# Performance work log

Measured on AMD Instinct MI355X. Metric: run time of the kernel, lower is better.

Reference implementation:

```python
import jax, jax.numpy as jnp
import numpy as np

H = 256
K = 16
EPS_LN = 1e-5


def setup_inputs() -> dict:
    key = jax.random.key(0)
    ks = jax.random.split(key, 24)
    B, N = 64, 256
    s = lambda *sh: 1.0 / np.sqrt(sh[0])
    inp = {
        "feat": jax.random.normal(ks[0], (B, N, H), jnp.float32),
        "centers": jax.random.normal(ks[1], (B, N, 3), jnp.float32),
        "text_global": jax.random.normal(ks[2], (B, H), jnp.float32),
        # geom_mlp: Linear(4,H) -> ReLU -> Linear(H,H) -> ReLU
        "w_geom1": jax.random.normal(ks[3], (4, H), jnp.float32) * s(4),
        "b_geom1": jnp.zeros((H,), jnp.float32),
        "w_geom2": jax.random.normal(ks[4], (H, H), jnp.float32) * s(H),
        "b_geom2": jnp.zeros((H,), jnp.float32),
        # text gate / bias projections
        "w_gate": jax.random.normal(ks[5], (H, H), jnp.float32) * s(H),
        "b_gate": jnp.zeros((H,), jnp.float32),
        "w_tbias": jax.random.normal(ks[6], (H, H), jnp.float32) * s(H),
        "b_tbias": jnp.zeros((H,), jnp.float32),
        # edge_mlp: Linear(H,H//2) -> ReLU -> Linear(H//2,1)
        "w_edge1": jax.random.normal(ks[7], (H, H // 2), jnp.float32) * s(H),
        "b_edge1": jnp.zeros((H // 2,), jnp.float32),
        "w_edge2": jax.random.normal(ks[8], (H // 2, 1), jnp.float32) * s(H // 2),
        "b_edge2": jnp.zeros((1,), jnp.float32),
        # msg_mlp: Linear(H,H) -> ReLU
        "w_msg": jax.random.normal(ks[9], (H, H), jnp.float32) * s(H),
        "b_msg": jnp.zeros((H,), jnp.float32),
        # out_proj: Linear(2H,H) -> ReLU
        "w_out": jax.random.normal(ks[10], (2 * H, H), jnp.float32) * s(2 * H),
        "b_out": jnp.zeros((H,), jnp.float32),
        # LayerNorm params
        "ln_gamma": jnp.ones((H,), jnp.float32),
        "ln_beta": jnp.zeros((H,), jnp.float32),
    }
    return inp


def _forward(feat, centers, text_global,
             w_geom1, b_geom1, w_geom2, b_geom2,
             w_gate, b_gate, w_tbias, b_tbias,
             w_edge1, b_edge1, w_edge2, b_edge2,
             w_msg, b_msg, w_out, b_out, ln_gamma, ln_beta):
    B, N, Hd = feat.shape
    k = min(K, N)
    # pairwise euclidean distances (B,N,N)
    sq = jnp.sum(centers * centers, axis=-1)  # (B,N)
    d2 = sq[:, :, None] + sq[:, None, :] - 2.0 * jnp.einsum('bnc,bmc->bnm', centers, centers)
    dist_matrix = jnp.sqrt(jnp.maximum(d2, 0.0))
    # k smallest -> top_k of negated distances (sorted ascending in distance)
    _, knn_idx = jax.lax.top_k(-dist_matrix, k)  # (B,N,k)
    idx_flat = knn_idx.reshape(B, N * k)
    feat_neigh = jnp.take_along_axis(feat, idx_flat[:, :, None], axis=1).reshape(B, N, k, Hd)
    centers_neigh = jnp.take_along_axis(centers, idx_flat[:, :, None], axis=1).reshape(B, N, k, 3)
    rel = centers_neigh - centers[:, :, None, :]  # (B,N,k,3)
    dist = jnp.linalg.norm(rel, axis=-1, keepdims=True) + 1e-6
    geom = jnp.concatenate([rel, jnp.log1p(dist)], axis=-1)  # (B,N,k,4)
    geom_emb = jax.nn.relu(jax.nn.relu(geom @ w_geom1 + b_geom1) @ w_geom2 + b_geom2)
    text_gate = jax.nn.sigmoid(text_global @ w_gate + b_gate)[:, None, None, :]
    text_bias = (text_global @ w_tbias + b_tbias)[:, None, None, :]
    geom_cond = geom_emb * text_gate + text_bias
    edge_feat = jnp.tanh(feat[:, :, None, :] + feat_neigh + geom_cond)  # (B,N,k,H)
    edge_logits = (jax.nn.relu(edge_feat @ w_edge1 + b_edge1) @ w_edge2 + b_edge2)[..., 0]
    edge_alpha = jax.nn.softmax(edge_logits, axis=-1)[..., None]  # (B,N,k,1)
    msg = jax.nn.relu(feat_neigh @ w_msg + b_msg)
    ctx = jnp.sum(edge_alpha * msg, axis=2)  # (B,N,H)
    out = jax.nn.relu(jnp.concatenate([feat, ctx], axis=-1) @ w_out + b_out)
    x = feat + out
    mu = jnp.mean(x, axis=-1, keepdims=True)
    var = jnp.mean((x - mu) ** 2, axis=-1, keepdims=True)
    return (x - mu) / jnp.sqrt(var + EPS_LN) * ln_gamma + ln_beta


def reference(feat, centers, text_global,
              w_geom1, b_geom1, w_geom2, b_geom2,
              w_gate, b_gate, w_tbias, b_tbias,
              w_edge1, b_edge1, w_edge2, b_edge2,
              w_msg, b_msg, w_out, b_out, ln_gamma, ln_beta):
    return _forward(feat, centers, text_global,
                    w_geom1, b_geom1, w_geom2, b_geom2,
                    w_gate, b_gate, w_tbias, b_tbias,
                    w_edge1, b_edge1, w_edge2, b_edge2,
                    w_msg, b_msg, w_out, b_out, ln_gamma, ln_beta)
```

## Files before the change

kernel.cpp:

```cpp
#include <hip/hip_runtime.h>

#define H 256
#define KNN 16
#define NPT 256
#define BB 64

typedef unsigned short u16;
typedef unsigned int u32;
typedef __attribute__((ext_vector_type(8))) short shortx8;
typedef __attribute__((ext_vector_type(4))) float floatx4;

__device__ __forceinline__ u16 f2b(float f) {
    u32 u = __float_as_uint(f);
    u32 r = (u + 0x7fffu + ((u >> 16) & 1u)) >> 16;
    return (u16)r;
}

__device__ __forceinline__ float fast_tanh(float x) {
    float e = __builtin_amdgcn_exp2f(x * 2.88539008177793f);
    return 1.0f - 2.0f * __builtin_amdgcn_rcpf(e + 1.0f);
}

__global__ __launch_bounds__(256) void prep_kernel(
    const float* __restrict__ w2, const float* __restrict__ we1,
    const float* __restrict__ wm, const float* __restrict__ wo,
    u16* __restrict__ w2t, u16* __restrict__ we1t,
    u16* __restrict__ wmt, u16* __restrict__ wot) {
    int tid = blockIdx.x * 256 + threadIdx.x;
    if (tid < 65536) {
        int n = tid >> 8, k = tid & 255;
        w2t[tid] = f2b(w2[k * 256 + n]);
    } else if (tid < 98304) {
        int t = tid - 65536;
        int n = t >> 8, k = t & 255;
        we1t[t] = f2b(we1[k * 128 + n]);
    } else if (tid < 163840) {
        int t = tid - 98304;
        int n = t >> 8, k = t & 255;
        wmt[t] = f2b(wm[k * 256 + n]);
    } else if (tid < 294912) {
        int t = tid - 163840;
        int n = t >> 9, k = t & 511;
        wot[t] = f2b(wo[k * 256 + n]);
    }
}

__global__ __launch_bounds__(256) void knn_kernel(const float* __restrict__ centers,
                                                  int* __restrict__ knn) {
    __shared__ float cx[NPT], cy[NPT], cz[NPT], sq[NPT];
    __shared__ float dl[4][64][17];
    __shared__ int il[4][64][17];
    int blk = blockIdx.x;
    int b = blk >> 2, n0 = (blk & 3) * 64;
    int h = threadIdx.x;
    int s = h >> 6, pt = h & 63;
    {
        const float* cb = centers + (size_t)b * NPT * 3;
        float x = cb[h * 3 + 0], y = cb[h * 3 + 1], z = cb[h * 3 + 2];
        cx[h] = x; cy[h] = y; cz[h] = z;
        sq[h] = x * x + y * y + z * z;
    }
    __syncthreads();
    int n = n0 + pt;
    float x = cx[n], y = cy[n], z = cz[n], sn = sq[n];
    float bd[KNN];
    int bi[KNN];
#pragma unroll
    for (int j = 0; j < KNN; j++) { bd[j] = 1e30f; bi[j] = 0x7fffffff; }
    for (int mm = 0; mm < 64; mm++) {
        int m = s * 64 + mm;
        float dot = x * cx[m] + y * cy[m] + z * cz[m];
        float d2 = (sn + sq[m]) - 2.0f * dot;
        float d = sqrtf(fmaxf(d2, 0.0f));
        if (d < bd[KNN - 1]) {
            bd[KNN - 1] = d; bi[KNN - 1] = m;
#pragma unroll
            for (int p = KNN - 1; p > 0; --p) {
                if (bd[p - 1] > bd[p]) {
                    float td = bd[p - 1]; bd[p - 1] = bd[p]; bd[p] = td;
                    int ti = bi[p - 1]; bi[p - 1] = bi[p]; bi[p] = ti;
                }
            }
        }
    }
#pragma unroll
    for (int j = 0; j < KNN; j++) { dl[s][pt][j] = bd[j]; il[s][pt][j] = bi[j]; }
    __syncthreads();
    if (s == 0) {
        float md[KNN];
        int mi[KNN];
#pragma unroll
        for (int j = 0; j < KNN; j++) { md[j] = dl[0][pt][j]; mi[j] = il[0][pt][j]; }
        for (int t = 1; t < 4; t++) {
            for (int j = 0; j < KNN; j++) {
                float d = dl[t][pt][j];
                int idx = il[t][pt][j];
                bool ins = (d < md[KNN - 1]) || (d == md[KNN - 1] && idx < mi[KNN - 1]);
                if (!ins) break;
                md[KNN - 1] = d; mi[KNN - 1] = idx;
#pragma unroll
                for (int p = KNN - 1; p > 0; --p) {
                    bool sw = (md[p - 1] > md[p]) ||
                              (md[p - 1] == md[p] && mi[p - 1] > mi[p]);
                    if (sw) {
                        float td = md[p - 1]; md[p - 1] = md[p]; md[p] = td;
                        int ti = mi[p - 1]; mi[p - 1] = mi[p]; mi[p] = ti;
                    }
                }
            }
        }
        int* kp = knn + (b * NPT + n0 + pt) * KNN;
#pragma unroll
        for (int j = 0; j < KNN; j++) kp[j] = mi[j];
    }
}

__global__ __launch_bounds__(512) void gate_kernel(const float* __restrict__ tg_g,
                                                   const float* __restrict__ wg,
                                                   const float* __restrict__ bg,
                                                   const float* __restrict__ wtb,
                                                   const float* __restrict__ btb,
                                                   float* __restrict__ gate,
                                                   float* __restrict__ tbias) {
    __shared__ float tg[H];
    int b = blockIdx.x, t = threadIdx.x;
    if (t < H) tg[t] = tg_g[b * H + t];
    __syncthreads();
    int h = t & 255;
    if (t < H) {
        float ag = bg[h];
#pragma unroll 4
        for (int i = 0; i < H; i++) ag += tg[i] * wg[i * H + h];
        gate[b * H + h] = 1.0f / (1.0f + expf(-ag));
    } else {
        float ab = btb[h];
#pragma unroll 4
        for (int i = 0; i < H; i++) ab += tg[i] * wtb[i * H + h];
        tbias[b * H + h] = ab;
    }
}

__global__ __launch_bounds__(256, 4) void msg_mfma(const float* __restrict__ feat,
                                                   const u16* __restrict__ wmt,
                                                   const float* __restrict__ bm,
                                                   float* __restrict__ MSG) {
    __shared__ __attribute__((aligned(16))) u16 A[64][264];
    int p0 = blockIdx.x * 64, h = threadIdx.x;
    int w = h >> 6, lane = h & 63, quad = lane >> 4, lq = lane & 15;
#pragma unroll 8
    for (int row = 0; row < 64; row++)
        A[row][h] = f2b(feat[(size_t)(p0 + row) * H + h]);
    __syncthreads();
    floatx4 acc[4][4];
#pragma unroll
    for (int rt = 0; rt < 4; rt++)
#pragma unroll
        for (int ct = 0; ct < 4; ct++) acc[rt][ct] = (floatx4){0, 0, 0, 0};
#pragma unroll 2
    for (int kt = 0; kt < 8; kt++) {
        shortx8 bf[4];
#pragma unroll
        for (int ct = 0; ct < 4; ct++)
            bf[ct] = *(const shortx8*)&wmt[(w * 64 + ct * 16 + lq) * 256 + kt * 32 + quad * 8];
#pragma unroll
        for (int rt = 0; rt < 4; rt++) {
            shortx8 a = *(const shortx8*)&A[rt * 16 + lq][kt * 32 + quad * 8];
#pragma unroll
            for (int ct = 0; ct < 4; ct++)
                acc[rt][ct] = __builtin_amdgcn_mfma_f32_16x16x32_bf16(a, bf[ct], acc[rt][ct], 0, 0, 0);
        }
    }
#pragma unroll
    for (int ct = 0; ct < 4; ct++) {
        int col = w * 64 + ct * 16 + lq;
        float bmc = bm[col];
#pragma unroll
        for (int rt = 0; rt < 4; rt++)
#pragma unroll
            for (int r = 0; r < 4; r++) {
                int row = rt * 16 + quad * 4 + r;
                MSG[(size_t)(p0 + row) * H + col] = fmaxf(acc[rt][ct][r] + bmc, 0.0f);
            }
    }
}

__global__ __launch_bounds__(256, 4) void edge_mfma(
    const float* __restrict__ feat, const float* __restrict__ centers,
    const float* __restrict__ w1, const float* __restrict__ b1,
    const u16* __restrict__ w2t, const float* __restrict__ b2v,
    const u16* __restrict__ we1t, const float* __restrict__ be1,
    const float* __restrict__ we2, const float* __restrict__ be2,
    const int* __restrict__ knn, const float* __restrict__ gateG,
    const float* __restrict__ tbiasG, const float* __restrict__ MSG,
    float* __restrict__ ctxG) {
    __shared__ __attribute__((aligned(16))) u16 A[64][264];
    __shared__ float fnS[4][H];
    __shared__ __attribute__((aligned(16))) float geomS[64][4];
    __shared__ int nidxS[64];
    __shared__ float part[4][64];
    __shared__ float logitsS[64];
    __shared__ float alphaS[64];

    int bn0 = blockIdx.x * 4;
    int b = bn0 >> 8, n0 = bn0 & 255;
    int h = threadIdx.x;
    int w = h >> 6, lane = h & 63, quad = lane >> 4, lq = lane & 15;

    if (h < 64) nidxS[h] = knn[bn0 * KNN + h];
#pragma unroll
    for (int p = 0; p < 4; p++)
        fnS[p][h] = feat[(size_t)(bn0 + p) * H + h];
    __syncthreads();

    if (h < 64) {
        int p = h >> 4;
        int m = nidxS[h];
        int n = n0 + p;
        const float* cb = centers + (size_t)b * NPT * 3;
        float rx = cb[m * 3 + 0] - cb[n * 3 + 0];
        float ry = cb[m * 3 + 1] - cb[n * 3 + 1];
        float rz = cb[m * 3 + 2] - cb[n * 3 + 2];
        float dist = sqrtf(rx * rx + ry * ry + rz * rz) + 1e-6f;
        geomS[h][0] = rx; geomS[h][1] = ry; geomS[h][2] = rz;
        geomS[h][3] = log1pf(dist);
    }
    __syncthreads();

    {
        float c0 = w1[h], c1 = w1[H + h], c2 = w1[2 * H + h], c3 = w1[3 * H + h];
        float bb = b1[h];
#pragma unroll 8
        for (int row = 0; row < 64; row++) {
            float4 g = *(const float4*)&geomS[row][0];
            float v = fmaxf(bb + g.x * c0 + g.y * c1 + g.z * c2 + g.w * c3, 0.0f);
            A[row][h] = f2b(v);
        }
    }
    __syncthreads();

    floatx4 acc[4][4];
#pragma unroll
    for (int rt = 0; rt < 4; rt++)
#pragma unroll
        for (int ct = 0; ct < 4; ct++) acc[rt][ct] = (floatx4){0, 0, 0, 0};
#pragma unroll 2
    for (int kt = 0; kt < 8; kt++) {
        shortx8 bf[4];
#pragma unroll
        for (int ct = 0; ct < 4; ct++)
            bf[ct] = *(const shortx8*)&w2t[(w * 64 + ct * 16 + lq) * 256 + kt * 32 + quad * 8];
#pragma unroll
        for (int rt = 0; rt < 4; rt++) {
            shortx8 a = *(const shortx8*)&A[rt * 16 + lq][kt * 32 + quad * 8];
#pragma unroll
            for (int ct = 0; ct < 4; ct++)
                acc[rt][ct] = __builtin_amdgcn_mfma_f32_16x16x32_bf16(a, bf[ct], acc[rt][ct], 0, 0, 0);
        }
    }
    __syncthreads();

#pragma unroll
    for (int ct = 0; ct < 4; ct++) {
        int col = w * 64 + ct * 16 + lq;
        float b2c = b2v[col];
        float gc = gateG[b * H + col];
        float tc = tbiasG[b * H + col];
#pragma unroll
        for (int rt = 0; rt < 4; rt++) {
            float fnc = fnS[rt][col];
#pragma unroll
            for (int r = 0; r < 4; r++) {
                int row = rt * 16 + quad * 4 + r;
                float fb = feat[((size_t)b * NPT + nidxS[row]) * H + col];
                float emb = fmaxf(acc[rt][ct][r] + b2c, 0.0f);
                float ef = fast_tanh(fnc + fb + emb * gc + tc);
                A[row][col] = f2b(ef);
            }
        }
    }
    __syncthreads();

    floatx4 acc2[4][2];
#pragma unroll
    for (int rt = 0; rt < 4; rt++)
#pragma unroll
        for (int c2 = 0; c2 < 2; c2++) acc2[rt][c2] = (floatx4){0, 0, 0, 0};
#pragma unroll 2
    for (int kt = 0; kt < 8; kt++) {
        shortx8 bf[2];
#pragma unroll
        for (int c2 = 0; c2 < 2; c2++)
            bf[c2] = *(const shortx8*)&we1t[(w * 32 + c2 * 16 + lq) * 256 + kt * 32 + quad * 8];
#pragma unroll
        for (int rt = 0; rt < 4; rt++) {
            shortx8 a = *(const shortx8*)&A[rt * 16 + lq][kt * 32 + quad * 8];
#pragma unroll
            for (int c2 = 0; c2 < 2; c2++)
                acc2[rt][c2] = __builtin_amdgcn_mfma_f32_16x16x32_bf16(a, bf[c2], acc2[rt][c2], 0, 0, 0);
        }
    }

    float pl[4][4];
#pragma unroll
    for (int rt = 0; rt < 4; rt++)
#pragma unroll
        for (int r = 0; r < 4; r++) pl[rt][r] = 0.0f;
#pragma unroll
    for (int c2 = 0; c2 < 2; c2++) {
        int col = w * 32 + c2 * 16 + lq;
        float be1c = be1[col], w2c = we2[col];
#pragma unroll
        for (int rt = 0; rt < 4; rt++)
#pragma unroll
            for (int r = 0; r < 4; r++)
                pl[rt][r] += fmaxf(acc2[rt][c2][r] + be1c, 0.0f) * w2c;
    }
#pragma unroll
    for (int d = 1; d < 16; d <<= 1)
#pragma unroll
        for (int rt = 0; rt < 4; rt++)
#pragma unroll
            for (int r = 0; r < 4; r++) pl[rt][r] += __shfl_xor(pl[rt][r], d, 16);
    if (lq == 0) {
#pragma unroll
        for (int rt = 0; rt < 4; rt++)
#pragma unroll
            for (int r = 0; r < 4; r++)
                part[w][rt * 16 + quad * 4 + r] = pl[rt][r];
    }
    __syncthreads();
    if (h < 64)
        logitsS[h] = part[0][h] + part[1][h] + part[2][h] + part[3][h] + be2[0];
    __syncthreads();
    if (h < 64) {
        int base = (h >> 4) * 16;
        float mx = -1e30f;
#pragma unroll
        for (int j = 0; j < KNN; j++) mx = fmaxf(mx, logitsS[base + j]);
        float sum = 0.0f;
#pragma unroll
        for (int j = 0; j < KNN; j++) sum += expf(logitsS[base + j] - mx);
        alphaS[h] = expf(logitsS[h] - mx) / sum;
    }
    __syncthreads();

    float c[4] = {0, 0, 0, 0};
#pragma unroll 16
    for (int row = 0; row < 64; row++) {
        float al = alphaS[row];
        c[row >> 4] += al * MSG[((size_t)b * NPT + nidxS[row]) * H + h];
    }
#pragma unroll
    for (int p = 0; p < 4; p++)
        ctxG[(size_t)(bn0 + p) * H + h] = c[p];
}

__global__ __launch_bounds__(256, 4) void out_mfma(const float* __restrict__ feat,
                                                   const float* __restrict__ ctxG,
                                                   const u16* __restrict__ wot,
                                                   const float* __restrict__ bo,
                                                   const float* __restrict__ gamma,
                                                   const float* __restrict__ beta,
                                                   float* __restrict__ out) {
    __shared__ __attribute__((aligned(16))) u16 A[32][520];
    __shared__ float redS[4][32], redS2[4][32];
    int p0 = blockIdx.x * 32, h = threadIdx.x;
    int w = h >> 6, lane = h & 63, quad = lane >> 4, lq = lane & 15;
#pragma unroll 8
    for (int row = 0; row < 32; row++) {
        A[row][h]       = f2b(feat[(size_t)(p0 + row) * H + h]);
        A[row][256 + h] = f2b(ctxG[(size_t)(p0 + row) * H + h]);
    }
    __syncthreads();
    floatx4 acc[2][4];
#pragma unroll
    for (int rt = 0; rt < 2; rt++)
#pragma unroll
        for (int ct = 0; ct < 4; ct++) acc[rt][ct] = (floatx4){0, 0, 0, 0};
#pragma unroll 2
    for (int kt = 0; kt < 16; kt++) {
        shortx8 bf[4];
#pragma unroll
        for (int ct = 0; ct < 4; ct++)
            bf[ct] = *(const shortx8*)&wot[(w * 64 + ct * 16 + lq) * 512 + kt * 32 + quad * 8];
#pragma unroll
        for (int rt = 0; rt < 2; rt++) {
            shortx8 a = *(const shortx8*)&A[rt * 16 + lq][kt * 32 + quad * 8];
#pragma unroll
            for (int ct = 0; ct < 4; ct++)
                acc[rt][ct] = __builtin_amdgcn_mfma_f32_16x16x32_bf16(a, bf[ct], acc[rt][ct], 0, 0, 0);
        }
    }
    float x[2][4][4];
    float sm[2][4], sq2[2][4];
#pragma unroll
    for (int rt = 0; rt < 2; rt++)
#pragma unroll
        for (int r = 0; r < 4; r++) { sm[rt][r] = 0.0f; sq2[rt][r] = 0.0f; }
#pragma unroll
    for (int rt = 0; rt < 2; rt++)
#pragma unroll
        for (int ct = 0; ct < 4; ct++) {
            int col = w * 64 + ct * 16 + lq;
            float boc = bo[col];
#pragma unroll
            for (int r = 0; r < 4; r++) {
                int row = rt * 16 + quad * 4 + r;
                float xx = feat[(size_t)(p0 + row) * H + col] +
                           fmaxf(acc[rt][ct][r] + boc, 0.0f);
                x[rt][ct][r] = xx;
                sm[rt][r] += xx;
                sq2[rt][r] += xx * xx;
            }
        }
#pragma unroll
    for (int d = 1; d < 16; d <<= 1)
#pragma unroll
        for (int rt = 0; rt < 2; rt++)
#pragma unroll
            for (int r = 0; r < 4; r++) {
                sm[rt][r] += __shfl_xor(sm[rt][r], d, 16);
                sq2[rt][r] += __shfl_xor(sq2[rt][r], d, 16);
            }
    if (lq == 0) {
#pragma unroll
        for (int rt = 0; rt < 2; rt++)
#pragma unroll
            for (int r = 0; r < 4; r++) {
                redS[w][rt * 16 + quad * 4 + r] = sm[rt][r];
                redS2[w][rt * 16 + quad * 4 + r] = sq2[rt][r];
            }
    }
    __syncthreads();
#pragma unroll
    for (int rt = 0; rt < 2; rt++)
#pragma unroll
        for (int r = 0; r < 4; r++) {
            int row = rt * 16 + quad * 4 + r;
            float s1 = redS[0][row] + redS[1][row] + redS[2][row] + redS[3][row];
            float s2 = redS2[0][row] + redS2[1][row] + redS2[2][row] + redS2[3][row];
            float mu = s1 * (1.0f / H);
            float var = s2 * (1.0f / H) - mu * mu;
            float inv = rsqrtf(fmaxf(var, 0.0f) + 1e-5f);
#pragma unroll
            for (int ct = 0; ct < 4; ct++) {
                int col = w * 64 + ct * 16 + lq;
                out[(size_t)(p0 + row) * H + col] =
                    (x[rt][ct][r] - mu) * inv * gamma[col] + beta[col];
            }
        }
}

extern "C" void kernel_launch(void* const* d_in, const int* in_sizes, int n_in,
                              void* d_out, int out_size, void* d_ws, size_t ws_size,
                              hipStream_t stream) {
    const float* feat    = (const float*)d_in[0];
    const float* centers = (const float*)d_in[1];
    const float* textg   = (const float*)d_in[2];
    const float* w1      = (const float*)d_in[3];
    const float* b1      = (const float*)d_in[4];
    const float* w2      = (const float*)d_in[5];
    const float* b2      = (const float*)d_in[6];
    const float* wg      = (const float*)d_in[7];
    const float* bg      = (const float*)d_in[8];
    const float* wtb     = (const float*)d_in[9];
    const float* btb     = (const float*)d_in[10];
    const float* we1     = (const float*)d_in[11];
    const float* be1     = (const float*)d_in[12];
    const float* we2     = (const float*)d_in[13];
    const float* be2     = (const float*)d_in[14];
    const float* wm      = (const float*)d_in[15];
    const float* bm      = (const float*)d_in[16];
    const float* wo      = (const float*)d_in[17];
    const float* bo      = (const float*)d_in[18];
    const float* gamma   = (const float*)d_in[19];
    const float* beta    = (const float*)d_in[20];

    char* ws = (char*)d_ws;
    size_t off = 0;
    int* knn     = (int*)(ws + off);   off += (size_t)BB * NPT * KNN * 4;
    float* gate  = (float*)(ws + off); off += (size_t)BB * H * 4;
    float* tbias = (float*)(ws + off); off += (size_t)BB * H * 4;
    float* MSG   = (float*)(ws + off); off += (size_t)BB * NPT * H * 4;
    float* ctxG  = (float*)(ws + off); off += (size_t)BB * NPT * H * 4;
    u16* w2t     = (u16*)(ws + off);   off += (size_t)256 * 256 * 2;
    u16* we1t    = (u16*)(ws + off);   off += (size_t)128 * 256 * 2;
    u16* wmt     = (u16*)(ws + off);   off += (size_t)256 * 256 * 2;
    u16* wot     = (u16*)(ws + off);   off += (size_t)256 * 512 * 2;

    prep_kernel<<<1152, 256, 0, stream>>>(w2, we1, wm, wo, w2t, we1t, wmt, wot);
    knn_kernel<<<256, 256, 0, stream>>>(centers, knn);
    gate_kernel<<<BB, 512, 0, stream>>>(textg, wg, bg, wtb, btb, gate, tbias);
    msg_mfma<<<BB * NPT / 64, 256, 0, stream>>>(feat, wmt, bm, MSG);
    edge_mfma<<<BB * NPT / 4, 256, 0, stream>>>(feat, centers, w1, b1, w2t, b2,
                                                we1t, be1, we2, be2, knn, gate, tbias,
                                                MSG, ctxG);
    out_mfma<<<BB * NPT / 32, 256, 0, stream>>>(feat, ctxG, wot, bo, gamma, beta,
                                                (float*)d_out);
}
```

Measured before the change: 365.9 us.

## Compute geom layer-1 with MFMA, vectorize neighbor aggregation, drop a barrier

The first geometry MLP layer (4 inputs plus bias) now runs as a padded bf16 MFMA against a pre-transposed w1/b1 matrix built in the prep kernel, replacing 64 scalar FMA rows per thread. The bias is folded in through a constant 1.0 input column. The context aggregation over neighbours now has each thread own one point and four channels, using float4 loads of MSG. One redundant __syncthreads is also removed. Geometry inputs are rounded to bf16 before layer 1, which adds some precision loss.

```diff
diff --git a/kernel.cpp b/kernel.cpp
--- a/kernel.cpp
+++ b/kernel.cpp
@@ -24,8 +24,9 @@
 __global__ __launch_bounds__(256) void prep_kernel(
     const float* __restrict__ w2, const float* __restrict__ we1,
     const float* __restrict__ wm, const float* __restrict__ wo,
+    const float* __restrict__ w1, const float* __restrict__ b1,
     u16* __restrict__ w2t, u16* __restrict__ we1t,
-    u16* __restrict__ wmt, u16* __restrict__ wot) {
+    u16* __restrict__ wmt, u16* __restrict__ wot, u16* __restrict__ w1t) {
     int tid = blockIdx.x * 256 + threadIdx.x;
     if (tid < 65536) {
         int n = tid >> 8, k = tid & 255;
@@ -42,6 +43,11 @@
         int t = tid - 163840;
         int n = t >> 9, k = t & 511;
         wot[t] = f2b(wo[k * 256 + n]);
+    } else {
+        int t = tid - 294912;
+        int n = t >> 5, k = t & 31;
+        float v = (k < 4) ? w1[k * 256 + n] : (k == 4 ? b1[n] : 0.0f);
+        w1t[t] = f2b(v);
     }
 }
 
@@ -186,7 +192,7 @@
 
 __global__ __launch_bounds__(256, 4) void edge_mfma(
     const float* __restrict__ feat, const float* __restrict__ centers,
-    const float* __restrict__ w1, const float* __restrict__ b1,
+    const u16* __restrict__ w1t,
     const u16* __restrict__ w2t, const float* __restrict__ b2v,
     const u16* __restrict__ we1t, const float* __restrict__ be1,
     const float* __restrict__ we2, const float* __restrict__ be2,
@@ -210,8 +216,6 @@
 #pragma unroll
     for (int p = 0; p < 4; p++)
         fnS[p][h] = feat[(size_t)(bn0 + p) * H + h];
-    __syncthreads();
-
     if (h < 64) {
         int p = h >> 4;
         int m = nidxS[h];
@@ -227,13 +231,30 @@
     __syncthreads();
 
     {
-        float c0 = w1[h], c1 = w1[H + h], c2 = w1[2 * H + h], c3 = w1[3 * H + h];
-        float bb = b1[h];
-#pragma unroll 8
-        for (int row = 0; row < 64; row++) {
-            float4 g = *(const float4*)&geomS[row][0];
-            float v = fmaxf(bb + g.x * c0 + g.y * c1 + g.z * c2 + g.w * c3, 0.0f);
-            A[row][h] = f2b(v);
+        shortx8 bw1[4];
+#pragma unroll
+        for (int ct = 0; ct < 4; ct++)
+            bw1[ct] = *(const shortx8*)&w1t[(w * 64 + ct * 16 + lq) * 32 + quad * 8];
+#pragma unroll
+        for (int rt = 0; rt < 4; rt++) {
+            shortx8 ag = {0, 0, 0, 0, 0, 0, 0, 0};
+            if (quad == 0) {
+                float4 g = *(const float4*)&geomS[rt * 16 + lq][0];
+                ag[0] = (short)f2b(g.x);
+                ag[1] = (short)f2b(g.y);
+                ag[2] = (short)f2b(g.z);
+                ag[3] = (short)f2b(g.w);
+                ag[4] = (short)0x3F80;
+            }
+#pragma unroll
+            for (int ct = 0; ct < 4; ct++) {
+                floatx4 accg = __builtin_amdgcn_mfma_f32_16x16x32_bf16(
+                    ag, bw1[ct], (floatx4){0, 0, 0, 0}, 0, 0, 0);
+#pragma unroll
+                for (int r = 0; r < 4; r++)
+                    A[rt * 16 + quad * 4 + r][w * 64 + ct * 16 + lq] =
+                        f2b(fmaxf(accg[r], 0.0f));
+            }
         }
     }
     __syncthreads();
@@ -344,15 +365,17 @@
     }
     __syncthreads();
 
-    float c[4] = {0, 0, 0, 0};
-#pragma unroll 16
-    for (int row = 0; row < 64; row++) {
-        float al = alphaS[row];
-        c[row >> 4] += al * MSG[((size_t)b * NPT + nidxS[row]) * H + h];
-    }
-#pragma unroll
-    for (int p = 0; p < 4; p++)
-        ctxG[(size_t)(bn0 + p) * H + h] = c[p];
+    {
+        int p = h >> 6, cg = (h & 63) * 4;
+        float4 c = {0, 0, 0, 0};
+#pragma unroll
+        for (int j = 0; j < KNN; j++) {
+            float al = alphaS[p * 16 + j];
+            float4 m = *(const float4*)&MSG[((size_t)b * NPT + nidxS[p * 16 + j]) * H + cg];
+            c.x += al * m.x; c.y += al * m.y; c.z += al * m.z; c.w += al * m.w;
+        }
+        *(float4*)&ctxG[(size_t)(bn0 + p) * H + cg] = c;
+    }
 }
 
 __global__ __launch_bounds__(256, 4) void out_mfma(const float* __restrict__ feat,
@@ -487,12 +510,14 @@
     u16* we1t    = (u16*)(ws + off);   off += (size_t)128 * 256 * 2;
     u16* wmt     = (u16*)(ws + off);   off += (size_t)256 * 256 * 2;
     u16* wot     = (u16*)(ws + off);   off += (size_t)256 * 512 * 2;
-
-    prep_kernel<<<1152, 256, 0, stream>>>(w2, we1, wm, wo, w2t, we1t, wmt, wot);
+    u16* w1t     = (u16*)(ws + off);   off += (size_t)256 * 32 * 2;
+
+    prep_kernel<<<1184, 256, 0, stream>>>(w2, we1, wm, wo, w1, b1,
+                                          w2t, we1t, wmt, wot, w1t);
     knn_kernel<<<256, 256, 0, stream>>>(centers, knn);
     gate_kernel<<<BB, 512, 0, stream>>>(textg, wg, bg, wtb, btb, gate, tbias);
     msg_mfma<<<BB * NPT / 64, 256, 0, stream>>>(feat, wmt, bm, MSG);
-    edge_mfma<<<BB * NPT / 4, 256, 0, stream>>>(feat, centers, w1, b1, w2t, b2,
+    edge_mfma<<<BB * NPT / 4, 256, 0, stream>>>(feat, centers, w1t, w2t, b2,
                                                 we1t, be1, we2, be2, knn, gate, tbias,
                                                 MSG, ctxG);
     out_mfma<<<BB * NPT / 32, 256, 0, stream>>>(feat, ctxG, wot, bo, gamma, beta,
```

Result: faster. 354.0 us (-3.3%).
